# Performance work log

Hardware: AMD Instinct MI355X
Metric: run time of the kernel (lower is better)

The kernel has to match this reference:

```python
import jax, jax.numpy as jnp
import numpy as np
import itertools

WS = (4, 4, 4, 2, 2)          # window size per dim
SS = (2, 2, 2, 1, 1)          # shift size per dim
B, D, H, W, U, V, C = 1, 16, 16, 8, 8, 8, 128
HEADS = 4
HD = C // HEADS
N = WS[0] * WS[1] * WS[2] * WS[3] * WS[4]   # 256 tokens per window


def _partition(x):
    # (b, D,H,W,U,V, c) -> (b*nW, N, c)
    b, c = x.shape[0], x.shape[-1]
    x = x.reshape(b, D // WS[0], WS[0], H // WS[1], WS[1], W // WS[2], WS[2],
                  U // WS[3], WS[3], V // WS[4], WS[4], c)
    x = x.transpose(0, 1, 3, 5, 7, 9, 2, 4, 6, 8, 10, 11)
    return x.reshape(-1, N, c)


def _reverse(win, b):
    # (b*nW, N, c) -> (b, D,H,W,U,V, c)
    c = win.shape[-1]
    x = win.reshape(b, D // WS[0], H // WS[1], W // WS[2], U // WS[3], V // WS[4],
                    WS[0], WS[1], WS[2], WS[3], WS[4], c)
    x = x.transpose(0, 1, 6, 2, 7, 3, 8, 4, 9, 5, 10, 11)
    return x.reshape(b, D, H, W, U, V, c)


def _ln(x, w, b, eps=1e-5):
    mu = jnp.mean(x, -1, keepdims=True)
    xc = x - mu
    var = jnp.mean(xc * xc, -1, keepdims=True)
    return xc * jax.lax.rsqrt(var + eps) * w + b


def _compute_mask():
    # 5D generalization of Swin's compute_mask: region labels then pairwise diff
    img = np.zeros((1, D, H, W, U, V, 1), np.float32)
    slcs = [[slice(0, -w), slice(-w, -s), slice(-s, None)] for w, s in zip(WS, SS)]
    cnt = 0
    for idx in itertools.product(*slcs):
        img[(slice(None),) + idx] = cnt
        cnt += 1
    mw = np.asarray(_partition(jnp.asarray(img))).squeeze(-1)  # (nW, N)
    diff = mw[:, None, :] - mw[:, :, None]
    return jnp.asarray(np.where(diff != 0, -1e9, 0.0).astype(np.float32))


def setup_inputs() -> dict:
    key = jax.random.key(0)
    ks = jax.random.split(key, 6)
    s = 0.02
    return {
        "x": jax.random.normal(ks[0], (B, D, H, W, U, V, C), jnp.float32),
        "mask": _compute_mask(),  # (512, 256, 256)
        "qkv_w": jax.random.normal(ks[1], (3 * C, C), jnp.float32) * s,
        "qkv_b": jnp.zeros((3 * C,), jnp.float32),
        "proj_w": jax.random.normal(ks[2], (C, C), jnp.float32) * s,
        "proj_b": jnp.zeros((C,), jnp.float32),
        "norm1_w": jnp.ones((C,), jnp.float32),
        "norm1_b": jnp.zeros((C,), jnp.float32),
        "norm2_w": jnp.ones((C,), jnp.float32),
        "norm2_b": jnp.zeros((C,), jnp.float32),
        "fc1_w": jax.random.normal(ks[3], (4 * C, C), jnp.float32) * s,
        "fc1_b": jnp.zeros((4 * C,), jnp.float32),
        "fc2_w": jax.random.normal(ks[4], (C, 4 * C), jnp.float32) * s,
        "fc2_b": jnp.zeros((C,), jnp.float32),
    }


def reference(x, mask, qkv_w, qkv_b, proj_w, proj_b, norm1_w, norm1_b,
              norm2_w, norm2_b, fc1_w, fc1_b, fc2_w, fc2_b):
    shortcut = x
    h = _ln(x, norm1_w, norm1_b)
    # cyclic shift
    h = jnp.roll(h, shift=tuple(-s for s in SS), axis=(1, 2, 3, 4, 5))
    win = _partition(h)                                # (nW, N, C)
    nw = win.shape[0]
    qkv = win @ qkv_w.T + qkv_b                        # (nW, N, 3C)
    qkv = qkv.reshape(nw, N, 3, HEADS, HD).transpose(2, 0, 3, 1, 4)
    q, k, v = qkv[0] * (HD ** -0.5), qkv[1], qkv[2]    # (nW, heads, N, hd)
    logits = jnp.einsum('bhnc,bhmc->bhnm', q, k) + mask[:, None]
    attn = jax.nn.softmax(logits, axis=-1)
    o = jnp.einsum('bhnm,bhmc->bhnc', attn, v)
    o = o.transpose(0, 2, 1, 3).reshape(nw, N, C)
    o = o @ proj_w.T + proj_b
    h = _reverse(o, B)
    # reverse cyclic shift
    h = jnp.roll(h, shift=SS, axis=(1, 2, 3, 4, 5))
    x = shortcut + h
    m = _ln(x, norm2_w, norm2_b)
    m = jax.nn.gelu(m @ fc1_w.T + fc1_b, approximate=False)
    m = m @ fc2_w.T + fc2_b
    return x + m
```

## Files before the change

kernel.cpp:

```cpp
#include <hip/hip_runtime.h>
#include <math.h>

typedef short bf16x8 __attribute__((ext_vector_type(8)));
typedef float f32x4 __attribute__((ext_vector_type(4)));
typedef unsigned short ushort_t;
typedef unsigned int uint_t;

__device__ __forceinline__ float bf2f(ushort_t h) { return __uint_as_float(((uint_t)h) << 16); }
__device__ __forceinline__ ushort_t f2bf(float f) {
    uint_t u = __float_as_uint(f);
    u += 0x7fffu + ((u >> 16) & 1u);
    return (ushort_t)(u >> 16);
}
__device__ __forceinline__ float bflo(uint_t u) { return __uint_as_float(u << 16); }
__device__ __forceinline__ float bfhi(uint_t u) { return __uint_as_float(u & 0xffff0000u); }

__device__ __forceinline__ bool probe_f32(const void* ones) {
    return ((const ushort_t*)ones)[0] == 0;
}

__device__ __forceinline__ void load8f(const void* p, size_t idx, bool f32, float* o) {
    if (f32) {
        const float4* q = (const float4*)((const float*)p + idx);
        float4 a = q[0], b = q[1];
        o[0] = a.x; o[1] = a.y; o[2] = a.z; o[3] = a.w;
        o[4] = b.x; o[5] = b.y; o[6] = b.z; o[7] = b.w;
    } else {
        uint4 u = *(const uint4*)((const ushort_t*)p + idx);
        o[0] = bflo(u.x); o[1] = bfhi(u.x); o[2] = bflo(u.y); o[3] = bfhi(u.y);
        o[4] = bflo(u.z); o[5] = bfhi(u.z); o[6] = bflo(u.w); o[7] = bfhi(u.w);
    }
}

__device__ __forceinline__ float load1(const void* p, size_t i, bool f32) {
    return f32 ? ((const float*)p)[i] : bf2f(((const ushort_t*)p)[i]);
}
__device__ __forceinline__ void store1(void* p, size_t i, bool f32, float v) {
    if (f32) ((float*)p)[i] = v;
    else ((ushort_t*)p)[i] = f2bf(v);
}

__device__ __forceinline__ float gelu_f(float x) {
    float ax = fabsf(x) * 0.70710678118654752f;
    float t = __builtin_amdgcn_rcpf(1.f + 0.3275911f * ax);
    float p = t * (0.254829592f +
              t * (-0.284496736f +
              t * (1.421413741f +
              t * (-1.453152027f +
              t * 1.061405429f))));
    float e = __expf(-ax * ax);
    float erfv = 1.f - p * e;
    float phi = 0.5f * (1.f + copysignf(erfv, x));
    return x * phi;
}

__device__ __forceinline__ void token_g(int t, int g[5]) {
    int n = t & 255, w = t >> 8;
    int wv = w & 3, wu = (w >> 2) & 3, ww = (w >> 4) & 1, wh = (w >> 5) & 3, wd = (w >> 7) & 3;
    int iv = n & 1, iu = (n >> 1) & 1, iw = (n >> 2) & 3, ih = (n >> 4) & 3, id = (n >> 6) & 3;
    g[0] = wd * 4 + id;
    g[1] = wh * 4 + ih;
    g[2] = ww * 4 + iw;
    g[3] = wu * 2 + iu;
    g[4] = wv * 2 + iv;
}

__device__ __forceinline__ int token_shiftpix(int t) {
    int g[5];
    token_g(t, g);
    int d = (g[0] + 2) & 15, h = (g[1] + 2) & 15, w = (g[2] + 2) & 7;
    int u = (g[3] + 1) & 7, v = (g[4] + 1) & 7;
    return ((((d * 16 + h) * 8 + w) * 8 + u) * 8 + v);
}

__device__ __forceinline__ int token_label(int t) {
    int g[5];
    token_g(t, g);
    int r0 = g[0] < 12 ? 0 : (g[0] < 14 ? 1 : 2);
    int r1 = g[1] < 12 ? 0 : (g[1] < 14 ? 1 : 2);
    int r2 = g[2] < 4 ? 0 : (g[2] < 6 ? 1 : 2);
    int r3 = g[3] < 6 ? 0 : (g[3] < 7 ? 1 : 2);
    int r4 = g[4] < 6 ? 0 : (g[4] < 7 ? 1 : 2);
    return (((r0 * 3 + r1) * 3 + r2) * 3 + r3) * 3 + r4;
}

#define MFMA16(a, b, c) __builtin_amdgcn_mfma_f32_16x16x32_bf16(a, b, c, 0, 0, 0)

#define QW_N 49152
#define PW_N 16384
#define W1_N 65536
#define W2_N 65536

__global__ __launch_bounds__(256) void k_prep(const void* __restrict__ qw,
                                              const void* __restrict__ pw,
                                              const void* __restrict__ w1,
                                              const void* __restrict__ w2,
                                              const void* __restrict__ probe,
                                              ushort_t* __restrict__ out) {
    const bool f32 = probe_f32(probe);
    size_t e = ((size_t)blockIdx.x * 256 + threadIdx.x) * 8;
    float v[8];
    size_t dst;
    if (e < QW_N) {
        load8f(qw, e, f32, v);
        int n = (int)(e >> 7), k = (int)(e & 127);
        int chunk = ((n >> 4) * 4 + (k >> 5)) * 64 + ((k >> 3) & 3) * 16 + (n & 15);
        dst = (size_t)chunk * 8;
    } else if (e < QW_N + PW_N) {
        size_t off = e - QW_N;
        load8f(pw, off, f32, v);
        int n = (int)(off >> 7), k = (int)(off & 127);
        int chunk = ((n >> 4) * 4 + (k >> 5)) * 64 + ((k >> 3) & 3) * 16 + (n & 15);
        dst = (size_t)QW_N + (size_t)chunk * 8;
    } else if (e < QW_N + PW_N + W1_N) {
        size_t off = e - (QW_N + PW_N);
        load8f(w1, off, f32, v);
        int n = (int)(off >> 7), k = (int)(off & 127);
        int chunk = ((n >> 4) * 4 + (k >> 5)) * 64 + ((k >> 3) & 3) * 16 + (n & 15);
        dst = (size_t)(QW_N + PW_N) + (size_t)chunk * 8;
    } else {
        size_t off = e - (QW_N + PW_N + W1_N);
        load8f(w2, off, f32, v);
        int n = (int)(off >> 9), k = (int)(off & 511);
        int chunk = ((n >> 4) * 16 + (k >> 5)) * 64 + ((k >> 3) & 3) * 16 + (n & 15);
        dst = (size_t)(QW_N + PW_N + W1_N) + (size_t)chunk * 8;
    }
    union { uint4 q; ushort_t u[8]; } pk;
#pragma unroll
    for (int j = 0; j < 8; j++) pk.u[j] = f2bf(v[j]);
    *reinterpret_cast<uint4*>(out + dst) = pk.q;
}

__global__ __launch_bounds__(256) void k_qkv(const void* __restrict__ x,
                                             const void* __restrict__ n1w,
                                             const void* __restrict__ n1b,
                                             const ushort_t* __restrict__ qwF,
                                             const void* __restrict__ qb,
                                             ushort_t* __restrict__ qT,
                                             ushort_t* __restrict__ kT,
                                             ushort_t* __restrict__ vF) {
    __shared__ __align__(16) ushort_t sA[64][136];
    const bool f32 = probe_f32(n1w);
    const int tid = threadIdx.x;
    const int rt = blockIdx.x;

    {
        int i = tid >> 2, q4 = tid & 3;
        int t = rt * 64 + i;
        int pix = token_shiftpix(t);
        float v[32];
        float s1 = 0.f, s2 = 0.f;
#pragma unroll
        for (int j = 0; j < 4; j++) {
            load8f(x, (size_t)pix * 128 + q4 * 32 + j * 8, f32, &v[j * 8]);
#pragma unroll
            for (int e = 0; e < 8; e++) { float f = v[j * 8 + e]; s1 += f; s2 += f * f; }
        }
        s1 += __shfl_xor(s1, 1);
        s2 += __shfl_xor(s2, 1);
        s1 += __shfl_xor(s1, 2);
        s2 += __shfl_xor(s2, 2);
        float mean = s1 * (1.f / 128.f);
        float var = s2 * (1.f / 128.f) - mean * mean;
        float rstd = rsqrtf(fmaxf(var, 0.f) + 1e-5f);
#pragma unroll
        for (int j = 0; j < 4; j++) {
            float wv[8], bv[8];
            load8f(n1w, q4 * 32 + j * 8, f32, wv);
            load8f(n1b, q4 * 32 + j * 8, f32, bv);
            union { uint4 q; ushort_t u[8]; } pk;
#pragma unroll
            for (int e = 0; e < 8; e++)
                pk.u[e] = f2bf((v[j * 8 + e] - mean) * rstd * wv[e] + bv[e]);
            *reinterpret_cast<uint4*>(&sA[i][q4 * 32 + j * 8]) = pk.q;
        }
    }
    __syncthreads();

    const int lane = tid & 63, wvid = tid >> 6, quad = lane >> 4, l16 = lane & 15;
    const int wbase4 = (rt >> 2) * 4;
    const int nadd = (rt & 3) * 64;

#pragma unroll 1
    for (int ct = 0; ct < 3; ct++) {
        f32x4 acc[4][2];
#pragma unroll
        for (int a = 0; a < 4; a++)
#pragma unroll
            for (int b = 0; b < 2; b++) acc[a][b] = (f32x4){0.f, 0.f, 0.f, 0.f};

#pragma unroll 2
        for (int k4 = 0; k4 < 4; k4++) {
            bf16x8 af[4], bg[2];
#pragma unroll
            for (int mi = 0; mi < 4; mi++)
                af[mi] = *reinterpret_cast<const bf16x8*>(&sA[mi * 16 + l16][k4 * 32 + quad * 8]);
#pragma unroll
            for (int ni = 0; ni < 2; ni++)
                bg[ni] = *reinterpret_cast<const bf16x8*>(
                    qwF + (size_t)(((ct * 8 + wvid * 2 + ni) * 4 + k4) * 64 + lane) * 8);
#pragma unroll
            for (int mi = 0; mi < 4; mi++)
#pragma unroll
                for (int ni = 0; ni < 2; ni++) acc[mi][ni] = MFMA16(af[mi], bg[ni], acc[mi][ni]);
        }
#pragma unroll
        for (int ni = 0; ni < 2; ni++) {
            int col = wvid * 32 + ni * 16 + l16;
            float bias = load1(qb, ct * 128 + col, f32);
            int h = col >> 5, d = col & 31;
            size_t whbase = (size_t)(wbase4 + h) * 8192;
#pragma unroll
            for (int mi = 0; mi < 4; mi++) {
#pragma unroll
                for (int r = 0; r < 4; r++) {
                    int row = mi * 16 + quad * 4 + r;
                    int n = nadd + row;
                    float val = acc[mi][ni][r] + bias;
                    if (ct == 0) {
                        qT[whbase + (size_t)n * 32 + d] = f2bf(val);
                    } else if (ct == 1) {
                        kT[whbase + (size_t)n * 32 + d] = f2bf(val);
                    } else {
                        size_t idx = whbase + (size_t)(n >> 5) * 1024 + (size_t)(d >> 4) * 512 +
                                     (size_t)((n >> 3) & 3) * 128 + (size_t)(d & 15) * 8 + (n & 7);
                        vF[idx] = f2bf(val);
                    }
                }
            }
        }
    }
}

__global__ __launch_bounds__(256) void k_attn(const ushort_t* __restrict__ qT,
                                              const ushort_t* __restrict__ kT,
                                              const ushort_t* __restrict__ vF,
                                              ushort_t* __restrict__ o) {
    __shared__ __align__(16) ushort_t sS[64][264];
    __shared__ unsigned char sLab[256];
    const int tid = threadIdx.x;
    const int rb = blockIdx.x, hh = blockIdx.y, w = blockIdx.z;
    const size_t whbase = (size_t)(w * 4 + hh) * 8192;

    sLab[tid] = (unsigned char)token_label(w * 256 + tid);
    __syncthreads();

    const int lane = tid & 63, wvid = tid >> 6, quad = lane >> 4, l16 = lane & 15;
    const int r0 = wvid * 16;

    bf16x8 aq = *reinterpret_cast<const bf16x8*>(
        qT + whbase + (size_t)(rb * 64 + r0 + l16) * 32 + quad * 8);

    f32x4 s[16];
    int myLab[4];
#pragma unroll
    for (int r = 0; r < 4; r++) myLab[r] = sLab[rb * 64 + r0 + quad * 4 + r];
#pragma unroll
    for (int ni = 0; ni < 16; ni++) {
        bf16x8 bk = *reinterpret_cast<const bf16x8*>(
            kT + whbase + (size_t)(ni * 16 + l16) * 32 + quad * 8);
        f32x4 c = (f32x4){0.f, 0.f, 0.f, 0.f};
        c = MFMA16(aq, bk, c);
        int klab = sLab[ni * 16 + l16];
#pragma unroll
        for (int r = 0; r < 4; r++)
            s[ni][r] = (klab == myLab[r]) ? c[r] * 0.17677669529663687f : -1.0e30f;
    }
    float mx[4], sm[4], inv[4];
#pragma unroll
    for (int r = 0; r < 4; r++) {
        float m2 = s[0][r];
#pragma unroll
        for (int ni = 1; ni < 16; ni++) m2 = fmaxf(m2, s[ni][r]);
        m2 = fmaxf(m2, __shfl_xor(m2, 1));
        m2 = fmaxf(m2, __shfl_xor(m2, 2));
        m2 = fmaxf(m2, __shfl_xor(m2, 4));
        m2 = fmaxf(m2, __shfl_xor(m2, 8));
        mx[r] = m2;
    }
#pragma unroll
    for (int r = 0; r < 4; r++) sm[r] = 0.f;
#pragma unroll
    for (int ni = 0; ni < 16; ni++) {
#pragma unroll
        for (int r = 0; r < 4; r++) {
            float p = __expf(s[ni][r] - mx[r]);
            s[ni][r] = p;
            sm[r] += p;
        }
    }
#pragma unroll
    for (int r = 0; r < 4; r++) {
        float t2 = sm[r];
        t2 += __shfl_xor(t2, 1);
        t2 += __shfl_xor(t2, 2);
        t2 += __shfl_xor(t2, 4);
        t2 += __shfl_xor(t2, 8);
        inv[r] = 1.f / t2;
    }
#pragma unroll
    for (int ni = 0; ni < 16; ni++) {
#pragma unroll
        for (int r = 0; r < 4; r++)
            sS[r0 + quad * 4 + r][ni * 16 + l16] = f2bf(s[ni][r]);
    }
    __syncthreads();

    f32x4 oacc[2];
    oacc[0] = (f32x4){0.f, 0.f, 0.f, 0.f};
    oacc[1] = (f32x4){0.f, 0.f, 0.f, 0.f};
#pragma unroll
    for (int kt = 0; kt < 8; kt++) {
        bf16x8 ap = *reinterpret_cast<const bf16x8*>(&sS[r0 + l16][kt * 32 + quad * 8]);
#pragma unroll
        for (int t2 = 0; t2 < 2; t2++) {
            bf16x8 bv = *reinterpret_cast<const bf16x8*>(
                vF + whbase + (size_t)((kt * 2 + t2) * 64 + lane) * 8);
            oacc[t2] = MFMA16(ap, bv, oacc[t2]);
        }
    }
#pragma unroll
    for (int t2 = 0; t2 < 2; t2++) {
#pragma unroll
        for (int r = 0; r < 4; r++) {
            int row = r0 + quad * 4 + r;
            int tok = w * 256 + rb * 64 + row;
            o[(size_t)tok * 128 + hh * 32 + t2 * 16 + l16] = f2bf(oacc[t2][r] * inv[r]);
        }
    }
}

__global__ __launch_bounds__(256) void k_proj(const ushort_t* __restrict__ o,
                                              const ushort_t* __restrict__ pwF,
                                              const void* __restrict__ pb,
                                              const void* __restrict__ x,
                                              const void* __restrict__ n1w,
                                              float* __restrict__ x2) {
    __shared__ __align__(16) ushort_t sA[128][136];
    __shared__ int sPix[128];
    const bool f32 = probe_f32(n1w);
    const int tid = threadIdx.x;
    const int rt = blockIdx.x;

    if (tid < 128) sPix[tid] = token_shiftpix(rt * 128 + tid);
    {
        int i = tid >> 1, half = tid & 1;
        const uint4* src = (const uint4*)(o + (size_t)(rt * 128 + i) * 128 + half * 64);
#pragma unroll
        for (int j = 0; j < 8; j++)
            *reinterpret_cast<uint4*>(&sA[i][half * 64 + j * 8]) = src[j];
    }
    __syncthreads();

    const int lane = tid & 63, wvid = tid >> 6;
    const int quad = lane >> 4, l16 = lane & 15;
    const int mbase = (wvid >> 1) * 64, nbase = (wvid & 1) * 64;
    const int tnb = (wvid & 1) * 4;
    f32x4 acc[4][4];
#pragma unroll
    for (int a = 0; a < 4; a++)
#pragma unroll
        for (int b = 0; b < 4; b++) acc[a][b] = (f32x4){0.f, 0.f, 0.f, 0.f};

#pragma unroll 2
    for (int k4 = 0; k4 < 4; k4++) {
        bf16x8 af[4], bg[4];
#pragma unroll
        for (int mi = 0; mi < 4; mi++)
            af[mi] = *reinterpret_cast<const bf16x8*>(&sA[mbase + mi * 16 + l16][k4 * 32 + quad * 8]);
#pragma unroll
        for (int ni = 0; ni < 4; ni++)
            bg[ni] = *reinterpret_cast<const bf16x8*>(
                pwF + (size_t)(((tnb + ni) * 4 + k4) * 64 + lane) * 8);
#pragma unroll
        for (int mi = 0; mi < 4; mi++)
#pragma unroll
            for (int ni = 0; ni < 4; ni++) acc[mi][ni] = MFMA16(af[mi], bg[ni], acc[mi][ni]);
    }
#pragma unroll
    for (int ni = 0; ni < 4; ni++) {
        int col = nbase + ni * 16 + l16;
        float bias = load1(pb, col, f32);
#pragma unroll
        for (int mi = 0; mi < 4; mi++) {
#pragma unroll
            for (int r = 0; r < 4; r++) {
                int row = mbase + mi * 16 + quad * 4 + r;
                int pix = sPix[row];
                size_t idx = (size_t)pix * 128 + col;
                x2[idx] = acc[mi][ni][r] + bias + load1(x, idx, f32);
            }
        }
    }
}

__global__ __launch_bounds__(256) void k_mlp(const float* __restrict__ x2,
                                             const void* __restrict__ n2w,
                                             const void* __restrict__ n2b,
                                             const ushort_t* __restrict__ w1f,
                                             const void* __restrict__ b1,
                                             const ushort_t* __restrict__ w2f,
                                             const void* __restrict__ b2,
                                             void* __restrict__ out) {
    __shared__ __align__(16) ushort_t sH[32][516];
    ushort_t (*sM)[136] = reinterpret_cast<ushort_t (*)[136]>(&sH[0][0]);
    const bool f32 = probe_f32(n2w);
    const int tid = threadIdx.x;
    const int t0 = blockIdx.x * 32;

    {
        int i = tid >> 3, oct = tid & 7;
        const float* row = x2 + (size_t)(t0 + i) * 128 + oct * 16;
        float v[16];
        float s1 = 0.f, s2 = 0.f;
#pragma unroll
        for (int j = 0; j < 4; j++) {
            float4 f = ((const float4*)row)[j];
            v[j * 4 + 0] = f.x; v[j * 4 + 1] = f.y; v[j * 4 + 2] = f.z; v[j * 4 + 3] = f.w;
            s1 += f.x + f.y + f.z + f.w;
            s2 += f.x * f.x + f.y * f.y + f.z * f.z + f.w * f.w;
        }
        s1 += __shfl_xor(s1, 1); s2 += __shfl_xor(s2, 1);
        s1 += __shfl_xor(s1, 2); s2 += __shfl_xor(s2, 2);
        s1 += __shfl_xor(s1, 4); s2 += __shfl_xor(s2, 4);
        float mean = s1 * (1.f / 128.f);
        float rstd = rsqrtf(fmaxf(s2 * (1.f / 128.f) - mean * mean, 0.f) + 1e-5f);
#pragma unroll
        for (int j = 0; j < 16; j++) {
            int c = oct * 16 + j;
            sM[i][c] = f2bf((v[j] - mean) * rstd * load1(n2w, c, f32) + load1(n2b, c, f32));
        }
    }
    __syncthreads();

    const int lane = tid & 63, wvid = tid >> 6, quad = lane >> 4, l16 = lane & 15;

    bf16x8 af[2][4];
#pragma unroll
    for (int mi = 0; mi < 2; mi++)
#pragma unroll
        for (int k4 = 0; k4 < 4; k4++)
            af[mi][k4] = *reinterpret_cast<const bf16x8*>(&sM[mi * 16 + l16][k4 * 32 + quad * 8]);
    __syncthreads();

    {
        const int cb = wvid * 128;
        bf16x8 wf[4], wn[4];
#pragma unroll
        for (int k4 = 0; k4 < 4; k4++)
            wf[k4] = *reinterpret_cast<const bf16x8*>(
                w1f + (size_t)(((wvid * 8) * 4 + k4) * 64 + lane) * 8);
#pragma unroll
        for (int ni = 0; ni < 8; ni++) {
            if (ni < 7) {
#pragma unroll
                for (int k4 = 0; k4 < 4; k4++)
                    wn[k4] = *reinterpret_cast<const bf16x8*>(
                        w1f + (size_t)(((wvid * 8 + ni + 1) * 4 + k4) * 64 + lane) * 8);
            }
            f32x4 a0 = (f32x4){0.f, 0.f, 0.f, 0.f};
            f32x4 a1 = (f32x4){0.f, 0.f, 0.f, 0.f};
#pragma unroll
            for (int k4 = 0; k4 < 4; k4++) {
                a0 = MFMA16(af[0][k4], wf[k4], a0);
                a1 = MFMA16(af[1][k4], wf[k4], a1);
            }
            int col = cb + ni * 16 + l16;
            float bias = load1(b1, col, f32);
#pragma unroll
            for (int r = 0; r < 4; r++) {
                sH[quad * 4 + r][col] = f2bf(gelu_f(a0[r] + bias));
                sH[16 + quad * 4 + r][col] = f2bf(gelu_f(a1[r] + bias));
            }
#pragma unroll
            for (int k4 = 0; k4 < 4; k4++) wf[k4] = wn[k4];
        }
    }
    __syncthreads();
    {
        const int cb = wvid * 32;
        float res[2][2][4];
#pragma unroll
        for (int mi = 0; mi < 2; mi++)
#pragma unroll
            for (int ni = 0; ni < 2; ni++)
#pragma unroll
                for (int r = 0; r < 4; r++)
                    res[mi][ni][r] = x2[(size_t)(t0 + mi * 16 + quad * 4 + r) * 128 + cb + ni * 16 + l16];
        f32x4 acc[2][2];
#pragma unroll
        for (int mi = 0; mi < 2; mi++)
#pragma unroll
            for (int ni = 0; ni < 2; ni++) acc[mi][ni] = (f32x4){0.f, 0.f, 0.f, 0.f};
        bf16x8 wf[2], wn[2];
#pragma unroll
        for (int ni = 0; ni < 2; ni++)
            wf[ni] = *reinterpret_cast<const bf16x8*>(
                w2f + (size_t)(((wvid * 2 + ni) * 16) * 64 + lane) * 8);
#pragma unroll
        for (int k0 = 0; k0 < 16; k0++) {
            if (k0 < 15) {
#pragma unroll
                for (int ni = 0; ni < 2; ni++)
                    wn[ni] = *reinterpret_cast<const bf16x8*>(
                        w2f + (size_t)(((wvid * 2 + ni) * 16 + k0 + 1) * 64 + lane) * 8);
            }
            bf16x8 a0 = *reinterpret_cast<const bf16x8*>(&sH[l16][k0 * 32 + quad * 8]);
            bf16x8 a1 = *reinterpret_cast<const bf16x8*>(&sH[16 + l16][k0 * 32 + quad * 8]);
            acc[0][0] = MFMA16(a0, wf[0], acc[0][0]);
            acc[1][0] = MFMA16(a1, wf[0], acc[1][0]);
            acc[0][1] = MFMA16(a0, wf[1], acc[0][1]);
            acc[1][1] = MFMA16(a1, wf[1], acc[1][1]);
            wf[0] = wn[0];
            wf[1] = wn[1];
        }
#pragma unroll
        for (int ni = 0; ni < 2; ni++) {
            int col = cb + ni * 16 + l16;
            float bias = load1(b2, col, f32);
#pragma unroll
            for (int mi = 0; mi < 2; mi++) {
#pragma unroll
                for (int r = 0; r < 4; r++) {
                    int row = mi * 16 + quad * 4 + r;
                    size_t idx = (size_t)(t0 + row) * 128 + col;
                    store1(out, idx, f32, acc[mi][ni][r] + bias + res[mi][ni][r]);
                }
            }
        }
    }
}

extern "C" void kernel_launch(void* const* d_in, const int* in_sizes, int n_in,
                              void* d_out, int out_size, void* d_ws, size_t ws_size,
                              hipStream_t stream) {
    (void)in_sizes; (void)n_in; (void)out_size; (void)ws_size;
    const void* x   = d_in[0];
    const void* qw  = d_in[2];
    const void* qb  = d_in[3];
    const void* pw  = d_in[4];
    const void* pb  = d_in[5];
    const void* n1w = d_in[6];
    const void* n1b = d_in[7];
    const void* n2w = d_in[8];
    const void* n2b = d_in[9];
    const void* w1  = d_in[10];
    const void* b1  = d_in[11];
    const void* w2  = d_in[12];
    const void* b2  = d_in[13];

    ushort_t* qT  = (ushort_t*)d_ws;
    ushort_t* kT  = (ushort_t*)((char*)d_ws + 33554432);
    ushort_t* vF  = (ushort_t*)((char*)d_ws + 67108864);
    ushort_t* ob  = (ushort_t*)((char*)d_ws + 100663296);
    float* x2     = (float*)d_ws;
    ushort_t* wts = (ushort_t*)((char*)d_ws + 134217728);
    ushort_t* qwF = wts;
    ushort_t* pwF = wts + QW_N;
    ushort_t* w1f = wts + QW_N + PW_N;
    ushort_t* w2f = wts + QW_N + PW_N + W1_N;

    hipLaunchKernelGGL(k_prep, dim3(96), dim3(256), 0, stream, qw, pw, w1, w2, n1w, wts);
    hipLaunchKernelGGL(k_qkv, dim3(2048), dim3(256), 0, stream, x, n1w, n1b, qwF, qb, qT, kT, vF);
    hipLaunchKernelGGL(k_attn, dim3(4, 4, 512), dim3(256), 0, stream, qT, kT, vF, ob);
    hipLaunchKernelGGL(k_proj, dim3(1024), dim3(256), 0, stream, ob, pwF, pb, x, n1w, x2);
    hipLaunchKernelGGL(k_mlp, dim3(4096), dim3(256), 0, stream, x2, n2w, n2b, w1f, b1, w2f, b2, d_out);
}
```

Baseline: 501.0 us.

## Split MLP hidden dimension into two halves to shrink LDS and registers

The fused MLP kernel now computes the 512-wide hidden layer in two 256-column passes. Each pass runs fc1+GELU into a smaller shared buffer and then accumulates its part of fc2, so LDS per block drops from about 33KB to about 25KB. Register-resident A fragments, the weight prefetch double-buffering and the early residual loads are removed, which lowers register pressure so more blocks can be resident per CU. In exchange, the kernel adds extra barriers and re-reads LDS inside the loops, and it loses the explicit weight prefetch.

New measurement: 522.8 us. 1.04x slower.

```diff
diff --git a/kernel.cpp b/kernel.cpp
--- a/kernel.cpp
+++ b/kernel.cpp
@@ -402,8 +402,8 @@
                                              const ushort_t* __restrict__ w2f,
                                              const void* __restrict__ b2,
                                              void* __restrict__ out) {
-    __shared__ __align__(16) ushort_t sH[32][516];
-    ushort_t (*sM)[136] = reinterpret_cast<ushort_t (*)[136]>(&sH[0][0]);
+    __shared__ __align__(16) ushort_t sM[32][136];
+    __shared__ __align__(16) ushort_t sH[32][264];
     const bool f32 = probe_f32(n2w);
     const int tid = threadIdx.x;
     const int t0 = blockIdx.x * 32;
@@ -435,85 +435,54 @@
 
     const int lane = tid & 63, wvid = tid >> 6, quad = lane >> 4, l16 = lane & 15;
 
-    bf16x8 af[2][4];
+    f32x4 acc[2][2];
 #pragma unroll
     for (int mi = 0; mi < 2; mi++)
 #pragma unroll
-        for (int k4 = 0; k4 < 4; k4++)
-            af[mi][k4] = *reinterpret_cast<const bf16x8*>(&sM[mi * 16 + l16][k4 * 32 + quad * 8]);
-    __syncthreads();
-
-    {
-        const int cb = wvid * 128;
-        bf16x8 wf[4], wn[4];
-#pragma unroll
-        for (int k4 = 0; k4 < 4; k4++)
-            wf[k4] = *reinterpret_cast<const bf16x8*>(
-                w1f + (size_t)(((wvid * 8) * 4 + k4) * 64 + lane) * 8);
-#pragma unroll
-        for (int ni = 0; ni < 8; ni++) {
-            if (ni < 7) {
-#pragma unroll
-                for (int k4 = 0; k4 < 4; k4++)
-                    wn[k4] = *reinterpret_cast<const bf16x8*>(
-                        w1f + (size_t)(((wvid * 8 + ni + 1) * 4 + k4) * 64 + lane) * 8);
-            }
+        for (int ni = 0; ni < 2; ni++) acc[mi][ni] = (f32x4){0.f, 0.f, 0.f, 0.f};
+
+#pragma unroll 1
+    for (int p = 0; p < 2; p++) {
+#pragma unroll 2
+        for (int ni = 0; ni < 4; ni++) {
+            const int tn = p * 16 + wvid * 4 + ni;
             f32x4 a0 = (f32x4){0.f, 0.f, 0.f, 0.f};
             f32x4 a1 = (f32x4){0.f, 0.f, 0.f, 0.f};
-#pragma unroll
+#pragma unroll 2
             for (int k4 = 0; k4 < 4; k4++) {
-                a0 = MFMA16(af[0][k4], wf[k4], a0);
-                a1 = MFMA16(af[1][k4], wf[k4], a1);
+                bf16x8 w = *reinterpret_cast<const bf16x8*>(
+                    w1f + (size_t)((tn * 4 + k4) * 64 + lane) * 8);
+                bf16x8 m0 = *reinterpret_cast<const bf16x8*>(&sM[l16][k4 * 32 + quad * 8]);
+                bf16x8 m1 = *reinterpret_cast<const bf16x8*>(&sM[16 + l16][k4 * 32 + quad * 8]);
+                a0 = MFMA16(m0, w, a0);
+                a1 = MFMA16(m1, w, a1);
             }
-            int col = cb + ni * 16 + l16;
-            float bias = load1(b1, col, f32);
+            int lcol = wvid * 64 + ni * 16 + l16;
+            float bias = load1(b1, p * 256 + lcol, f32);
 #pragma unroll
             for (int r = 0; r < 4; r++) {
-                sH[quad * 4 + r][col] = f2bf(gelu_f(a0[r] + bias));
-                sH[16 + quad * 4 + r][col] = f2bf(gelu_f(a1[r] + bias));
+                sH[quad * 4 + r][lcol] = f2bf(gelu_f(a0[r] + bias));
+                sH[16 + quad * 4 + r][lcol] = f2bf(gelu_f(a1[r] + bias));
             }
-#pragma unroll
-            for (int k4 = 0; k4 < 4; k4++) wf[k4] = wn[k4];
-        }
-    }
-    __syncthreads();
+        }
+        __syncthreads();
+#pragma unroll 2
+        for (int k0 = 0; k0 < 8; k0++) {
+            bf16x8 h0 = *reinterpret_cast<const bf16x8*>(&sH[l16][k0 * 32 + quad * 8]);
+            bf16x8 h1 = *reinterpret_cast<const bf16x8*>(&sH[16 + l16][k0 * 32 + quad * 8]);
+#pragma unroll
+            for (int ni = 0; ni < 2; ni++) {
+                bf16x8 w = *reinterpret_cast<const bf16x8*>(
+                    w2f + (size_t)(((wvid * 2 + ni) * 16 + p * 8 + k0) * 64 + lane) * 8);
+                acc[0][ni] = MFMA16(h0, w, acc[0][ni]);
+                acc[1][ni] = MFMA16(h1, w, acc[1][ni]);
+            }
+        }
+        __syncthreads();
+    }
+
     {
         const int cb = wvid * 32;
-        float res[2][2][4];
-#pragma unroll
-        for (int mi = 0; mi < 2; mi++)
-#pragma unroll
-            for (int ni = 0; ni < 2; ni++)
-#pragma unroll
-                for (int r = 0; r < 4; r++)
-                    res[mi][ni][r] = x2[(size_t)(t0 + mi * 16 + quad * 4 + r) * 128 + cb + ni * 16 + l16];
-        f32x4 acc[2][2];
-#pragma unroll
-        for (int mi = 0; mi < 2; mi++)
-#pragma unroll
-            for (int ni = 0; ni < 2; ni++) acc[mi][ni] = (f32x4){0.f, 0.f, 0.f, 0.f};
-        bf16x8 wf[2], wn[2];
-#pragma unroll
-        for (int ni = 0; ni < 2; ni++)
-            wf[ni] = *reinterpret_cast<const bf16x8*>(
-                w2f + (size_t)(((wvid * 2 + ni) * 16) * 64 + lane) * 8);
-#pragma unroll
-        for (int k0 = 0; k0 < 16; k0++) {
-            if (k0 < 15) {
-#pragma unroll
-                for (int ni = 0; ni < 2; ni++)
-                    wn[ni] = *reinterpret_cast<const bf16x8*>(
-                        w2f + (size_t)(((wvid * 2 + ni) * 16 + k0 + 1) * 64 + lane) * 8);
-            }
-            bf16x8 a0 = *reinterpret_cast<const bf16x8*>(&sH[l16][k0 * 32 + quad * 8]);
-            bf16x8 a1 = *reinterpret_cast<const bf16x8*>(&sH[16 + l16][k0 * 32 + quad * 8]);
-            acc[0][0] = MFMA16(a0, wf[0], acc[0][0]);
-            acc[1][0] = MFMA16(a1, wf[0], acc[1][0]);
-            acc[0][1] = MFMA16(a0, wf[1], acc[0][1]);
-            acc[1][1] = MFMA16(a1, wf[1], acc[1][1]);
-            wf[0] = wn[0];
-            wf[1] = wn[1];
-        }
 #pragma unroll
         for (int ni = 0; ni < 2; ni++) {
             int col = cb + ni * 16 + l16;
@@ -524,7 +493,7 @@
                 for (int r = 0; r < 4; r++) {
                     int row = mi * 16 + quad * 4 + r;
                     size_t idx = (size_t)(t0 + row) * 128 + col;
-                    store1(out, idx, f32, acc[mi][ni][r] + bias + res[mi][ni][r]);
+                    store1(out, idx, f32, acc[mi][ni][r] + bias + x2[idx]);
                 }
             }
         }
```
